# Kernel tuning notes

Measured on AMD Instinct MI355X. Metric: run time of the kernel, lower is better.

The kernel has to match this reference:

```python
import jax, jax.numpy as jnp
import numpy as np

NUM_HEADS = 8
NUM_POINTS = 4


def setup_inputs() -> dict:
    key = jax.random.key(0)
    bs, h, w = 2, 128, 128
    cin = cout = 256
    nq = h * w
    ks = jax.random.split(key, 6)
    query = jax.random.normal(ks[0], (bs, nq, cin), jnp.float32)
    value = jax.random.normal(ks[1], (bs, nq, cin), jnp.float32)
    # sampling_offsets: small random weight, bias = directional grid init (as in init_weights)
    W_off = jax.random.normal(ks[2], (cin, NUM_HEADS * NUM_POINTS * 2), jnp.float32) * 0.01
    thetas = np.arange(NUM_HEADS, dtype=np.float32) * (2.0 * np.pi / NUM_HEADS)
    grid = np.stack([np.cos(thetas), np.sin(thetas)], -1)
    grid = grid / np.abs(grid).max(-1, keepdims=True)
    grid = np.tile(grid[:, None, :], (1, NUM_POINTS, 1)) * (np.arange(NUM_POINTS, dtype=np.float32)[None, :, None] + 1.0)
    b_off = jnp.asarray(grid.reshape(-1), jnp.float32)
    W_attn = jax.random.normal(ks[3], (cin, NUM_HEADS * NUM_POINTS), jnp.float32) * 0.01
    b_attn = jnp.zeros((NUM_HEADS * NUM_POINTS,), jnp.float32)
    s = 1.0 / np.sqrt(cin)  # xavier-ish uniform
    W_val = jax.random.uniform(ks[4], (cin, cout), jnp.float32, -s, s)
    b_val = jnp.zeros((cout,), jnp.float32)
    W_out = jax.random.uniform(ks[5], (cout, cout), jnp.float32, -s, s)
    b_out = jnp.zeros((cout,), jnp.float32)
    return {"query": query, "value": value, "W_off": W_off, "b_off": b_off,
            "W_attn": W_attn, "b_attn": b_attn, "W_val": W_val, "b_val": b_val,
            "W_out": W_out, "b_out": b_out, "h": h, "w": w}


def _bilinear_sample(v_flat, ix, iy, h, w):
    # v_flat: (bs, heads, h*w, d); ix/iy: (bs, heads, nq, P) pixel coords.
    # grid_sample bilinear, align_corners=False, padding_mode='zeros'.
    x0 = jnp.floor(ix)
    y0 = jnp.floor(iy)
    wx1 = ix - x0
    wy1 = iy - y0
    bs, hd, nq, P = ix.shape
    acc = 0.0
    corners = ((x0, y0, (1.0 - wx1) * (1.0 - wy1)),
               (x0 + 1.0, y0, wx1 * (1.0 - wy1)),
               (x0, y0 + 1.0, (1.0 - wx1) * wy1),
               (x0 + 1.0, y0 + 1.0, wx1 * wy1))
    for xc, yc, wgt in corners:
        xi = xc.astype(jnp.int32)
        yi = yc.astype(jnp.int32)
        valid = (xi >= 0) & (xi < w) & (yi >= 0) & (yi < h)
        idx = jnp.clip(yi, 0, h - 1) * w + jnp.clip(xi, 0, w - 1)
        g = jnp.take_along_axis(v_flat, idx.reshape(bs, hd, nq * P)[..., None], axis=2)
        acc = acc + g.reshape(bs, hd, nq, P, -1) * (wgt * valid)[..., None]
    return acc  # (bs, heads, nq, P, d)


def deform_attn(query, value, W_off, b_off, W_attn, b_attn, W_val, b_val, h, w):
    bs, nq, _ = query.shape
    d = W_val.shape[1] // NUM_HEADS
    v = (value @ W_val + b_val).reshape(bs, nq, NUM_HEADS, d)
    off = (query @ W_off + b_off).reshape(bs, nq, NUM_HEADS, NUM_POINTS, 2)
    aw = jax.nn.softmax((query @ W_attn + b_attn).reshape(bs, nq, NUM_HEADS, NUM_POINTS), axis=-1)
    # reference points in [0,1], scale_ratio=1.0, (x, y) order
    ys = (jnp.arange(h, dtype=jnp.float32) + 0.5) / h
    xs = (jnp.arange(w, dtype=jnp.float32) + 0.5) / w
    ry, rx = jnp.meshgrid(ys, xs, indexing='ij')
    ref = jnp.stack([rx.reshape(-1), ry.reshape(-1)], -1)  # (nq, 2)
    loc = ref[None, :, None, None, :] + off / jnp.array([w, h], jnp.float32)
    grid = 2.0 * loc - 1.0  # normalized grid_sample coords
    grid = grid.transpose(0, 2, 1, 3, 4)  # (bs, heads, nq, P, 2)
    ix = (grid[..., 0] + 1.0) * (w / 2.0) - 0.5
    iy = (grid[..., 1] + 1.0) * (h / 2.0) - 0.5
    v_flat = v.transpose(0, 2, 1, 3)  # (bs, heads, h*w, d)
    sampled = _bilinear_sample(v_flat, ix, iy, h, w)  # (bs, heads, nq, P, d)
    out = (sampled * aw.transpose(0, 2, 1, 3)[..., None]).sum(3)  # (bs, heads, nq, d)
    return out.transpose(0, 2, 1, 3).reshape(bs, nq, NUM_HEADS * d)


def reference(query, value, W_off, b_off, W_attn, b_attn, W_val, b_val, W_out, b_out, h, w):
    attn = deform_attn(query, value, W_off, b_off, W_attn, b_attn, W_val, b_val, h, w)
    # dropout acts as identity in eval mode; identity residual = query
    return attn @ W_out + b_out + query
```

## Files before the change

### kernel.cpp

```cpp
#include <hip/hip_runtime.h>

#define H_IMG 128
#define W_IMG 128
#define NQ (H_IMG * W_IMG)
#define CIN 256
#define NH 8
#define NP 4
#define DH 32
#define LDSP 264

typedef __bf16 bf16x4 __attribute__((ext_vector_type(4)));
typedef __bf16 bf16x8 __attribute__((ext_vector_type(8)));
typedef float f32x4 __attribute__((ext_vector_type(4)));

__global__ __launch_bounds__(256) void prep_weights(
    const float* __restrict__ Wval, const float* __restrict__ Wout,
    const float* __restrict__ Woff, const float* __restrict__ Wattn,
    const float* __restrict__ boff, const float* __restrict__ battn,
    __bf16* __restrict__ btv, __bf16* __restrict__ bto,
    __bf16* __restrict__ btoa, float* __restrict__ bias96) {
  int id = blockIdx.x * 256 + threadIdx.x;
  if (id < 256 * 256) {
    int n = id >> 8, k = id & 255;
    btv[n * 256 + k] = (__bf16)Wval[k * 256 + n];
    bto[n * 256 + k] = (__bf16)Wout[k * 256 + n];
  }
  if (id < 96 * 256) {
    int n = id >> 8, k = id & 255;
    float w = (n < 64) ? Woff[k * 64 + n] : Wattn[k * 32 + (n - 64)];
    btoa[n * 256 + k] = (__bf16)w;
  }
  if (id < 96) {
    bias96[id] = (id < 64) ? boff[id] : battn[id - 64];
  }
}

__global__ __launch_bounds__(256) void gemm_v(
    const float* __restrict__ A, const __bf16* __restrict__ BT,
    const float* __restrict__ bias, __bf16* __restrict__ v, int M) {
  const int t = threadIdx.x;
  const int lane = t & 63;
  const int wave = t >> 6;
  const int r = lane & 15;
  const int q = lane >> 4;
  const int gm0 = blockIdx.x * 64;
  const int wn = wave * 64;

  __shared__ __bf16 As[64 * LDSP];

#pragma unroll
  for (int i = 0; i < 16; ++i) {
    int g = i * 256 + t;
    int row = g >> 6, c4 = g & 63;
    float4 f = *(const float4*)(A + (size_t)(gm0 + row) * 256 + c4 * 4);
    bf16x4 hh;
    hh[0] = (__bf16)f.x; hh[1] = (__bf16)f.y;
    hh[2] = (__bf16)f.z; hh[3] = (__bf16)f.w;
    *(bf16x4*)(&As[row * LDSP + c4 * 4]) = hh;
  }
  __syncthreads();

  f32x4 acc[4][4];
#pragma unroll
  for (int mt = 0; mt < 4; ++mt)
#pragma unroll
    for (int nt = 0; nt < 4; ++nt) acc[mt][nt] = (f32x4){0.f, 0.f, 0.f, 0.f};

#pragma unroll
  for (int kt = 0; kt < 8; ++kt) {
    const int ko = kt * 32 + q * 8;
    bf16x8 a[4], b[4];
#pragma unroll
    for (int mt = 0; mt < 4; ++mt)
      a[mt] = *(const bf16x8*)(&As[(mt * 16 + r) * LDSP + ko]);
#pragma unroll
    for (int nt = 0; nt < 4; ++nt)
      b[nt] = *(const bf16x8*)(BT + (size_t)(wn + nt * 16 + r) * 256 + ko);
#pragma unroll
    for (int mt = 0; mt < 4; ++mt)
#pragma unroll
      for (int nt = 0; nt < 4; ++nt)
        acc[mt][nt] =
            __builtin_amdgcn_mfma_f32_16x16x32_bf16(a[mt], b[nt], acc[mt][nt], 0, 0, 0);
  }

#pragma unroll
  for (int mt = 0; mt < 4; ++mt)
#pragma unroll
    for (int nt = 0; nt < 4; ++nt)
#pragma unroll
      for (int rr = 0; rr < 4; ++rr) {
        int row = gm0 + mt * 16 + q * 4 + rr;
        int col = wn + nt * 16 + r;
        v[((size_t)(col >> 5) * M + row) * 32 + (col & 31)] =
            (__bf16)(acc[mt][nt][rr] + bias[col]);
      }
}

__global__ __launch_bounds__(256) void oa_sample_out(
    const float* __restrict__ query, const __bf16* __restrict__ btoa,
    const float* __restrict__ bias96, const __bf16* __restrict__ v,
    const __bf16* __restrict__ bto, const float* __restrict__ b_out,
    float* __restrict__ out, int M) {
  const int t = threadIdx.x;
  const int lane = t & 63;
  const int wave = t >> 6;
  const int r = lane & 15;
  const int q = lane >> 4;
  const int gm0 = blockIdx.x * 64;

  __shared__ __bf16 As[64 * LDSP];
  __shared__ float oas[64 * 100];

#pragma unroll
  for (int i = 0; i < 16; ++i) {
    int g = i * 256 + t;
    int row = g >> 6, c4 = g & 63;
    float4 f = *(const float4*)(query + (size_t)(gm0 + row) * 256 + c4 * 4);
    bf16x4 hh;
    hh[0] = (__bf16)f.x; hh[1] = (__bf16)f.y;
    hh[2] = (__bf16)f.z; hh[3] = (__bf16)f.w;
    *(bf16x4*)(&As[row * LDSP + c4 * 4]) = hh;
  }
  __syncthreads();

  {
    const int wm = (wave & 1) * 32;
    const int n0 = (wave >> 1) * 48;
    f32x4 acc[2][3];
#pragma unroll
    for (int mt = 0; mt < 2; ++mt)
#pragma unroll
      for (int nt = 0; nt < 3; ++nt) acc[mt][nt] = (f32x4){0.f, 0.f, 0.f, 0.f};
#pragma unroll
    for (int kt = 0; kt < 8; ++kt) {
      const int ko = kt * 32 + q * 8;
      bf16x8 a0 = *(const bf16x8*)(&As[(wm + r) * LDSP + ko]);
      bf16x8 a1 = *(const bf16x8*)(&As[(wm + 16 + r) * LDSP + ko]);
      bf16x8 b[3];
#pragma unroll
      for (int nt = 0; nt < 3; ++nt)
        b[nt] = *(const bf16x8*)(btoa + (size_t)(n0 + nt * 16 + r) * 256 + ko);
#pragma unroll
      for (int nt = 0; nt < 3; ++nt) {
        acc[0][nt] = __builtin_amdgcn_mfma_f32_16x16x32_bf16(a0, b[nt], acc[0][nt], 0, 0, 0);
        acc[1][nt] = __builtin_amdgcn_mfma_f32_16x16x32_bf16(a1, b[nt], acc[1][nt], 0, 0, 0);
      }
    }
#pragma unroll
    for (int mt = 0; mt < 2; ++mt)
#pragma unroll
      for (int nt = 0; nt < 3; ++nt)
#pragma unroll
        for (int rr = 0; rr < 4; ++rr) {
          int rl = wm + mt * 16 + q * 4 + rr;
          int col = n0 + nt * 16 + r;
          oas[rl * 100 + col] = acc[mt][nt][rr] + bias96[col];
        }
  }
  __syncthreads();

  {
    const int qrow = t >> 2;
    const int c8 = (t & 3) * 8;
    const int row = gm0 + qrow;
    const int b = row >> 14;
    const int qi = row & (NQ - 1);
    const int x = qi & (W_IMG - 1);
    const int y = qi >> 7;
    const float* oar = &oas[qrow * 100];
#pragma unroll
    for (int h = 0; h < NH; ++h) {
      float l0 = oar[64 + h * 4 + 0];
      float l1 = oar[64 + h * 4 + 1];
      float l2 = oar[64 + h * 4 + 2];
      float l3 = oar[64 + h * 4 + 3];
      float mx = fmaxf(fmaxf(l0, l1), fmaxf(l2, l3));
      float e0 = __expf(l0 - mx), e1 = __expf(l1 - mx);
      float e2 = __expf(l2 - mx), e3 = __expf(l3 - mx);
      float inv = 1.f / (e0 + e1 + e2 + e3);
      float awp[4] = {e0 * inv, e1 * inv, e2 * inv, e3 * inv};
      float fa[8] = {0.f, 0.f, 0.f, 0.f, 0.f, 0.f, 0.f, 0.f};
      const __bf16* vh = v + ((size_t)h * M + (size_t)b * NQ) * 32 + c8;
#pragma unroll
      for (int p = 0; p < NP; ++p) {
        float ox = oar[h * 8 + p * 2 + 0];
        float oy = oar[h * 8 + p * 2 + 1];
        float ix = (float)x + ox;
        float iy = (float)y + oy;
        float x0f = floorf(ix), y0f = floorf(iy);
        float wx1 = ix - x0f, wy1 = iy - y0f;
        int x0 = (int)x0f, y0 = (int)y0f;
        float wgt[4] = {(1.f - wx1) * (1.f - wy1), wx1 * (1.f - wy1),
                        (1.f - wx1) * wy1, wx1 * wy1};
        int xs[4] = {x0, x0 + 1, x0, x0 + 1};
        int ysv[4] = {y0, y0, y0 + 1, y0 + 1};
#pragma unroll
        for (int c = 0; c < 4; ++c) {
          int xi = xs[c], yi = ysv[c];
          bool valid = (xi >= 0) & (xi < W_IMG) & (yi >= 0) & (yi < H_IMG);
          int xc = xi < 0 ? 0 : (xi > W_IMG - 1 ? W_IMG - 1 : xi);
          int yc = yi < 0 ? 0 : (yi > H_IMG - 1 ? H_IMG - 1 : yi);
          float wv = awp[p] * wgt[c] * (valid ? 1.f : 0.f);
          bf16x8 g = *(const bf16x8*)(vh + (size_t)(yc * W_IMG + xc) * 32);
#pragma unroll
          for (int j = 0; j < 8; ++j) fa[j] += wv * (float)g[j];
        }
      }
      bf16x8 o;
#pragma unroll
      for (int j = 0; j < 8; ++j) o[j] = (__bf16)fa[j];
      *(bf16x8*)(&As[qrow * LDSP + h * DH + c8]) = o;
    }
  }
  __syncthreads();

  {
    const int wn = wave * 64;
    f32x4 acc[4][4];
#pragma unroll
    for (int mt = 0; mt < 4; ++mt)
#pragma unroll
      for (int nt = 0; nt < 4; ++nt) acc[mt][nt] = (f32x4){0.f, 0.f, 0.f, 0.f};
#pragma unroll
    for (int kt = 0; kt < 8; ++kt) {
      const int ko = kt * 32 + q * 8;
      bf16x8 a[4], b[4];
#pragma unroll
      for (int mt = 0; mt < 4; ++mt)
        a[mt] = *(const bf16x8*)(&As[(mt * 16 + r) * LDSP + ko]);
#pragma unroll
      for (int nt = 0; nt < 4; ++nt)
        b[nt] = *(const bf16x8*)(bto + (size_t)(wn + nt * 16 + r) * 256 + ko);
#pragma unroll
      for (int mt = 0; mt < 4; ++mt)
#pragma unroll
        for (int nt = 0; nt < 4; ++nt)
          acc[mt][nt] =
              __builtin_amdgcn_mfma_f32_16x16x32_bf16(a[mt], b[nt], acc[mt][nt], 0, 0, 0);
    }
#pragma unroll
    for (int mt = 0; mt < 4; ++mt)
#pragma unroll
      for (int nt = 0; nt < 4; ++nt)
#pragma unroll
        for (int rr = 0; rr < 4; ++rr) {
          int row = gm0 + mt * 16 + q * 4 + rr;
          int col = wn + nt * 16 + r;
          out[(size_t)row * 256 + col] =
              acc[mt][nt][rr] + b_out[col] + query[(size_t)row * 256 + col];
        }
  }
}

extern "C" void kernel_launch(void* const* d_in, const int* in_sizes, int n_in,
                              void* d_out, int out_size, void* d_ws, size_t ws_size,
                              hipStream_t stream) {
  const float* query  = (const float*)d_in[0];
  const float* value  = (const float*)d_in[1];
  const float* W_off  = (const float*)d_in[2];
  const float* b_off  = (const float*)d_in[3];
  const float* W_attn = (const float*)d_in[4];
  const float* b_attn = (const float*)d_in[5];
  const float* W_val  = (const float*)d_in[6];
  const float* b_val  = (const float*)d_in[7];
  const float* W_out  = (const float*)d_in[8];
  const float* b_out  = (const float*)d_in[9];
  float* out = (float*)d_out;

  char* ws = (char*)d_ws;
  __bf16* btv    = (__bf16*)(ws + 0);
  __bf16* bto    = (__bf16*)(ws + 131072);
  __bf16* btoa   = (__bf16*)(ws + 262144);
  float*  bias96 = (float*)(ws + 311296);
  __bf16* v      = (__bf16*)(ws + 524288);

  const int M = in_sizes[0] / CIN;

  prep_weights<<<256, 256, 0, stream>>>(W_val, W_out, W_off, W_attn,
                                        b_off, b_attn, btv, bto, btoa, bias96);
  gemm_v<<<M / 64, 256, 0, stream>>>(value, btv, b_val, v, M);
  oa_sample_out<<<M / 64, 256, 0, stream>>>(query, btoa, bias96, v, bto, b_out, out, M);
}
```

Measured before the change: 166.5 us.

## Use 512 threads per block in fused sample kernel, one head per thread

The fused offset/attention GEMM + sampling + output projection kernel now runs 512 threads (8 waves) per 64-row block instead of 256, with each GEMM phase's tile split across more waves. In the sampling phase each thread handles one (query, head) pair and loads all 32 channels with four 16-byte loads per corner, instead of looping over 8 heads on an 8-channel slice. The goal is more latency hiding for the random gathers and more parallel work per block. In exchange each thread keeps 32 accumulators, which raises register pressure under the 512-thread launch bound, and each wave's gather addresses are spread more widely.

```diff
diff --git a/kernel.cpp b/kernel.cpp
--- a/kernel.cpp
+++ b/kernel.cpp
@@ -97,7 +97,7 @@
       }
 }
 
-__global__ __launch_bounds__(256) void oa_sample_out(
+__global__ __launch_bounds__(512, 4) void oa_sample_out(
     const float* __restrict__ query, const __bf16* __restrict__ btoa,
     const float* __restrict__ bias96, const __bf16* __restrict__ v,
     const __bf16* __restrict__ bto, const float* __restrict__ b_out,
@@ -113,8 +113,8 @@
   __shared__ float oas[64 * 100];
 
 #pragma unroll
-  for (int i = 0; i < 16; ++i) {
-    int g = i * 256 + t;
+  for (int i = 0; i < 8; ++i) {
+    int g = i * 512 + t;
     int row = g >> 6, c4 = g & 63;
     float4 f = *(const float4*)(query + (size_t)(gm0 + row) * 256 + c4 * 4);
     bf16x4 hh;
@@ -125,124 +125,131 @@
   __syncthreads();
 
   {
-    const int wm = (wave & 1) * 32;
-    const int n0 = (wave >> 1) * 48;
-    f32x4 acc[2][3];
-#pragma unroll
-    for (int mt = 0; mt < 2; ++mt)
-#pragma unroll
-      for (int nt = 0; nt < 3; ++nt) acc[mt][nt] = (f32x4){0.f, 0.f, 0.f, 0.f};
+    const int wm = (wave & 3) * 16;
+    const int n0 = (wave >> 2) * 48;
+    f32x4 acc[3];
+#pragma unroll
+    for (int nt = 0; nt < 3; ++nt) acc[nt] = (f32x4){0.f, 0.f, 0.f, 0.f};
 #pragma unroll
     for (int kt = 0; kt < 8; ++kt) {
       const int ko = kt * 32 + q * 8;
-      bf16x8 a0 = *(const bf16x8*)(&As[(wm + r) * LDSP + ko]);
-      bf16x8 a1 = *(const bf16x8*)(&As[(wm + 16 + r) * LDSP + ko]);
+      bf16x8 a = *(const bf16x8*)(&As[(wm + r) * LDSP + ko]);
       bf16x8 b[3];
 #pragma unroll
       for (int nt = 0; nt < 3; ++nt)
         b[nt] = *(const bf16x8*)(btoa + (size_t)(n0 + nt * 16 + r) * 256 + ko);
 #pragma unroll
-      for (int nt = 0; nt < 3; ++nt) {
-        acc[0][nt] = __builtin_amdgcn_mfma_f32_16x16x32_bf16(a0, b[nt], acc[0][nt], 0, 0, 0);
-        acc[1][nt] = __builtin_amdgcn_mfma_f32_16x16x32_bf16(a1, b[nt], acc[1][nt], 0, 0, 0);
+      for (int nt = 0; nt < 3; ++nt)
+        acc[nt] = __builtin_amdgcn_mfma_f32_16x16x32_bf16(a, b[nt], acc[nt], 0, 0, 0);
+    }
+#pragma unroll
+    for (int nt = 0; nt < 3; ++nt)
+#pragma unroll
+      for (int rr = 0; rr < 4; ++rr) {
+        int rl = wm + q * 4 + rr;
+        int col = n0 + nt * 16 + r;
+        oas[rl * 100 + col] = acc[nt][rr] + bias96[col];
       }
-    }
-#pragma unroll
-    for (int mt = 0; mt < 2; ++mt)
-#pragma unroll
-      for (int nt = 0; nt < 3; ++nt)
-#pragma unroll
-        for (int rr = 0; rr < 4; ++rr) {
-          int rl = wm + mt * 16 + q * 4 + rr;
-          int col = n0 + nt * 16 + r;
-          oas[rl * 100 + col] = acc[mt][nt][rr] + bias96[col];
-        }
   }
   __syncthreads();
 
   {
-    const int qrow = t >> 2;
-    const int c8 = (t & 3) * 8;
+    const int qrow = t >> 3;
+    const int h = t & 7;
     const int row = gm0 + qrow;
     const int b = row >> 14;
     const int qi = row & (NQ - 1);
     const int x = qi & (W_IMG - 1);
     const int y = qi >> 7;
     const float* oar = &oas[qrow * 100];
-#pragma unroll
-    for (int h = 0; h < NH; ++h) {
-      float l0 = oar[64 + h * 4 + 0];
-      float l1 = oar[64 + h * 4 + 1];
-      float l2 = oar[64 + h * 4 + 2];
-      float l3 = oar[64 + h * 4 + 3];
-      float mx = fmaxf(fmaxf(l0, l1), fmaxf(l2, l3));
-      float e0 = __expf(l0 - mx), e1 = __expf(l1 - mx);
-      float e2 = __expf(l2 - mx), e3 = __expf(l3 - mx);
-      float inv = 1.f / (e0 + e1 + e2 + e3);
-      float awp[4] = {e0 * inv, e1 * inv, e2 * inv, e3 * inv};
-      float fa[8] = {0.f, 0.f, 0.f, 0.f, 0.f, 0.f, 0.f, 0.f};
-      const __bf16* vh = v + ((size_t)h * M + (size_t)b * NQ) * 32 + c8;
-#pragma unroll
-      for (int p = 0; p < NP; ++p) {
-        float ox = oar[h * 8 + p * 2 + 0];
-        float oy = oar[h * 8 + p * 2 + 1];
-        float ix = (float)x + ox;
-        float iy = (float)y + oy;
-        float x0f = floorf(ix), y0f = floorf(iy);
-        float wx1 = ix - x0f, wy1 = iy - y0f;
-        int x0 = (int)x0f, y0 = (int)y0f;
-        float wgt[4] = {(1.f - wx1) * (1.f - wy1), wx1 * (1.f - wy1),
-                        (1.f - wx1) * wy1, wx1 * wy1};
-        int xs[4] = {x0, x0 + 1, x0, x0 + 1};
-        int ysv[4] = {y0, y0, y0 + 1, y0 + 1};
-#pragma unroll
-        for (int c = 0; c < 4; ++c) {
-          int xi = xs[c], yi = ysv[c];
-          bool valid = (xi >= 0) & (xi < W_IMG) & (yi >= 0) & (yi < H_IMG);
-          int xc = xi < 0 ? 0 : (xi > W_IMG - 1 ? W_IMG - 1 : xi);
-          int yc = yi < 0 ? 0 : (yi > H_IMG - 1 ? H_IMG - 1 : yi);
-          float wv = awp[p] * wgt[c] * (valid ? 1.f : 0.f);
-          bf16x8 g = *(const bf16x8*)(vh + (size_t)(yc * W_IMG + xc) * 32);
-#pragma unroll
-          for (int j = 0; j < 8; ++j) fa[j] += wv * (float)g[j];
+
+    float l0 = oar[64 + h * 4 + 0];
+    float l1 = oar[64 + h * 4 + 1];
+    float l2 = oar[64 + h * 4 + 2];
+    float l3 = oar[64 + h * 4 + 3];
+    float mx = fmaxf(fmaxf(l0, l1), fmaxf(l2, l3));
+    float e0 = __expf(l0 - mx), e1 = __expf(l1 - mx);
+    float e2 = __expf(l2 - mx), e3 = __expf(l3 - mx);
+    float inv = 1.f / (e0 + e1 + e2 + e3);
+    float awp[4] = {e0 * inv, e1 * inv, e2 * inv, e3 * inv};
+
+    float fa[32];
+#pragma unroll
+    for (int j = 0; j < 32; ++j) fa[j] = 0.f;
+
+    const __bf16* vh = v + ((size_t)h * M + (size_t)b * NQ) * 32;
+#pragma unroll
+    for (int p = 0; p < NP; ++p) {
+      float ox = oar[h * 8 + p * 2 + 0];
+      float oy = oar[h * 8 + p * 2 + 1];
+      float ix = (float)x + ox;
+      float iy = (float)y + oy;
+      float x0f = floorf(ix), y0f = floorf(iy);
+      float wx1 = ix - x0f, wy1 = iy - y0f;
+      int x0 = (int)x0f, y0 = (int)y0f;
+      float wgt[4] = {(1.f - wx1) * (1.f - wy1), wx1 * (1.f - wy1),
+                      (1.f - wx1) * wy1, wx1 * wy1};
+      int xs[4] = {x0, x0 + 1, x0, x0 + 1};
+      int ysv[4] = {y0, y0, y0 + 1, y0 + 1};
+#pragma unroll
+      for (int c = 0; c < 4; ++c) {
+        int xi = xs[c], yi = ysv[c];
+        bool valid = (xi >= 0) & (xi < W_IMG) & (yi >= 0) & (yi < H_IMG);
+        int xc = xi < 0 ? 0 : (xi > W_IMG - 1 ? W_IMG - 1 : xi);
+        int yc = yi < 0 ? 0 : (yi > H_IMG - 1 ? H_IMG - 1 : yi);
+        float wv = awp[p] * wgt[c] * (valid ? 1.f : 0.f);
+        const __bf16* src = vh + (size_t)(yc * W_IMG + xc) * 32;
+        bf16x8 g0 = *(const bf16x8*)(src);
+        bf16x8 g1 = *(const bf16x8*)(src + 8);
+        bf16x8 g2 = *(const bf16x8*)(src + 16);
+        bf16x8 g3 = *(const bf16x8*)(src + 24);
+#pragma unroll
+        for (int j = 0; j < 8; ++j) {
+          fa[j]      += wv * (float)g0[j];
+          fa[8 + j]  += wv * (float)g1[j];
+          fa[16 + j] += wv * (float)g2[j];
+          fa[24 + j] += wv * (float)g3[j];
         }
       }
+    }
+#pragma unroll
+    for (int jj = 0; jj < 4; ++jj) {
       bf16x8 o;
 #pragma unroll
-      for (int j = 0; j < 8; ++j) o[j] = (__bf16)fa[j];
-      *(bf16x8*)(&As[qrow * LDSP + h * DH + c8]) = o;
+      for (int j = 0; j < 8; ++j) o[j] = (__bf16)fa[jj * 8 + j];
+      *(bf16x8*)(&As[qrow * LDSP + h * DH + jj * 8]) = o;
     }
   }
   __syncthreads();
 
   {
-    const int wn = wave * 64;
-    f32x4 acc[4][4];
-#pragma unroll
-    for (int mt = 0; mt < 4; ++mt)
-#pragma unroll
-      for (int nt = 0; nt < 4; ++nt) acc[mt][nt] = (f32x4){0.f, 0.f, 0.f, 0.f};
+    const int wn = wave * 32;
+    f32x4 acc[4][2];
+#pragma unroll
+    for (int mt = 0; mt < 4; ++mt)
+#pragma unroll
+      for (int nt = 0; nt < 2; ++nt) acc[mt][nt] = (f32x4){0.f, 0.f, 0.f, 0.f};
 #pragma unroll
     for (int kt = 0; kt < 8; ++kt) {
       const int ko = kt * 32 + q * 8;
-      bf16x8 a[4], b[4];
+      bf16x8 a[4], b[2];
 #pragma unroll
       for (int mt = 0; mt < 4; ++mt)
         a[mt] = *(const bf16x8*)(&As[(mt * 16 + r) * LDSP + ko]);
 #pragma unroll
-      for (int nt = 0; nt < 4; ++nt)
+      for (int nt = 0; nt < 2; ++nt)
         b[nt] = *(const bf16x8*)(bto + (size_t)(wn + nt * 16 + r) * 256 + ko);
 #pragma unroll
       for (int mt = 0; mt < 4; ++mt)
 #pragma unroll
-        for (int nt = 0; nt < 4; ++nt)
+        for (int nt = 0; nt < 2; ++nt)
           acc[mt][nt] =
               __builtin_amdgcn_mfma_f32_16x16x32_bf16(a[mt], b[nt], acc[mt][nt], 0, 0, 0);
     }
 #pragma unroll
     for (int mt = 0; mt < 4; ++mt)
 #pragma unroll
-      for (int nt = 0; nt < 4; ++nt)
+      for (int nt = 0; nt < 2; ++nt)
 #pragma unroll
         for (int rr = 0; rr < 4; ++rr) {
           int row = gm0 + mt * 16 + q * 4 + rr;
@@ -280,5 +287,5 @@
   prep_weights<<<256, 256, 0, stream>>>(W_val, W_out, W_off, W_attn,
                                         b_off, b_attn, btv, bto, btoa, bias96);
   gemm_v<<<M / 64, 256, 0, stream>>>(value, btv, b_val, v, M);
-  oa_sample_out<<<M / 64, 256, 0, stream>>>(query, btoa, bias96, v, bto, b_out, out, M);
-}
+  oa_sample_out<<<M / 64, 512, 0, stream>>>(query, btoa, bias96, v, bto, b_out, out, M);
+}
```

Result: slower. 268.4 us (+61.2%).
